# Optimization experiments

Hardware: AMD Instinct MI355X
Metric: run time of the kernel (lower is better)

The kernel has to match this reference:

```python
import jax, jax.numpy as jnp
import numpy as np


def _conv(x, w, b):
    # 3x3 stride-1 pad-1 conv, NCHW / OIHW
    y = jax.lax.conv_general_dilated(x, w, (1, 1), 'SAME',
                                     dimension_numbers=('NCHW', 'OIHW', 'NCHW'))
    return y + b[None, :, None, None]


def _lrelu(x):
    return jax.nn.leaky_relu(x, negative_slope=0.2)


def setup_inputs() -> dict:
    key = jax.random.key(0)
    ks = jax.random.split(key, 12)
    B, H, W = 64, 32, 32
    C, K, DH, OUT = 16, 10, 256, 784

    def w(k, shape, fan_in):
        return jax.random.normal(k, shape, jnp.float32) / np.sqrt(fan_in)

    inp = {
        'x':   jax.random.normal(ks[0], (B, 1, H, W), jnp.float32),
        # encoder convs
        'cw1': w(ks[1], (C, 1, 3, 3), 1 * 9),   'cb1': jnp.zeros((C,), jnp.float32),
        'cw2': w(ks[2], (C, C, 3, 3), C * 9),   'cb2': jnp.zeros((C,), jnp.float32),
        # 2 residual blocks, 2 convs each
        'r1w1': w(ks[3], (C, C, 3, 3), C * 9), 'r1b1': jnp.zeros((C,), jnp.float32),
        'r1w2': w(ks[4], (C, C, 3, 3), C * 9), 'r1b2': jnp.zeros((C,), jnp.float32),
        'r2w1': w(ks[5], (C, C, 3, 3), C * 9), 'r2b1': jnp.zeros((C,), jnp.float32),
        'r2w2': w(ks[6], (C, C, 3, 3), C * 9), 'r2b2': jnp.zeros((C,), jnp.float32),
        # VQ codebook (k=10 hardcoded in source, d = encoder channels)
        'codebook': jax.random.normal(ks[7], (K, C), jnp.float32),
        # decoder MLP 16 -> 256 -> 256 -> 784 (torch Linear layout: [out, in])
        'dw1': w(ks[8], (DH, C), C),     'db1': jnp.zeros((DH,), jnp.float32),
        'dw2': w(ks[9], (DH, DH), DH),   'db2': jnp.zeros((DH,), jnp.float32),
        'dw3': w(ks[10], (OUT, DH), DH), 'db3': jnp.zeros((OUT,), jnp.float32),
    }
    return inp


def reference(x, cw1, cb1, cw2, cb2,
              r1w1, r1b1, r1w2, r1b2, r2w1, r2b1, r2w2, r2b2,
              codebook, dw1, db1, dw2, db2, dw3, db3):
    # ---- encoder ----
    h = _lrelu(_conv(x, cw1, cb1))
    h = _lrelu(_conv(h, cw2, cb2))
    h = _lrelu(_conv(_lrelu(_conv(h, r1w1, r1b1)), r1w2, r1b2)) + h  # ResBlock 1
    h = _lrelu(_conv(_lrelu(_conv(h, r2w1, r2b1)), r2w2, r2b2)) + h  # ResBlock 2
    z_e = h  # [B, C, H, W]

    # ---- VQ: cdist^2 + argmin + gather ----
    B, C, H, W = z_e.shape
    x_flat = z_e.transpose(0, 2, 3, 1).reshape(-1, C)          # [N, C]
    d2 = (jnp.sum(x_flat ** 2, axis=1, keepdims=True)
          + jnp.sum(codebook ** 2, axis=1)[None, :]
          - 2.0 * x_flat @ codebook.T)                          # [N, K]
    idx = jnp.argmin(d2, axis=1)                                # [N]
    z_q = codebook[idx].reshape(B, H, W, C).transpose(0, 3, 1, 2)
    # straight-through (as written in source: value == z_e, grad flows via z_q)
    z_st = z_q + jax.lax.stop_gradient(z_e - z_q)               # [B, C, H, W]

    # ---- decoder: per-pixel MLP 16 -> 256 -> 256 -> 784 ----
    g = z_st.transpose(0, 2, 3, 1)                              # [B, H, W, C]
    g = _lrelu(g @ dw1.T + db1)
    g = _lrelu(g @ dw2.T + db2)
    x_recon = jax.nn.sigmoid(g @ dw3.T + db3)                   # [B, H, W, 784]
    return x_recon, z_e, z_st, z_q
```

## Files before the change

kernel.cpp:

```cpp
#include <hip/hip_runtime.h>

typedef __attribute__((ext_vector_type(8))) short bfrag;
typedef __attribute__((ext_vector_type(4))) float ffrag;

__device__ __forceinline__ float lrelu(float x) { return x > 0.f ? x : 0.2f * x; }

__device__ __forceinline__ short f2b(float f) {
    union { float f; unsigned u; } x; x.f = f;
    unsigned r = x.u + 0x7fffu + ((x.u >> 16) & 1u);
    return (short)(r >> 16);
}

__global__ __launch_bounds__(256) void prep_k(
    const float* __restrict__ dw1, const float* __restrict__ dw2, const float* __restrict__ dw3,
    const float* __restrict__ cw1, const float* __restrict__ cw2,
    const float* __restrict__ r1w1, const float* __restrict__ r1w2,
    const float* __restrict__ r2w1, const float* __restrict__ r2w2,
    short* __restrict__ dw1p, short* __restrict__ dw2b, short* __restrict__ dw3b,
    float* __restrict__ wtr)
{
    const int i = blockIdx.x * 256 + threadIdx.x;
    if (i < 65536)  dw2b[i] = f2b(dw2[i]);
    if (i < 200704) dw3b[i] = f2b(dw3[i]);
    if (i < 8192) {
        const int row = i >> 5, k = i & 31;
        dw1p[i] = (k < 16) ? f2b(dw1[row * 16 + k]) : (short)0;
    }
    if (i < 2304) {
        const int co = i & 15;
        const int q  = i >> 4;
        const int k  = q % 9;
        const int ci = q / 9;
        const int src = (co * 16 + ci) * 9 + k;
        wtr[2304 * 1 + i] = cw2 [src];
        wtr[2304 * 2 + i] = r1w1[src];
        wtr[2304 * 3 + i] = r1w2[src];
        wtr[2304 * 4 + i] = r2w1[src];
        wtr[2304 * 5 + i] = r2w2[src];
        if (ci == 0) wtr[i] = cw1[co * 9 + k];
    }
}

template<int CIN, int RIN, int ROUT, int HOUT, bool HASRES, int RRES, int HRES>
__device__ __forceinline__ void conv_stage(
    const float* __restrict__ in, float* __restrict__ out, const float* __restrict__ res,
    const float* __restrict__ wt, const float* __restrict__ bias, int r0, int t)
{
    const int lo = (r0 - HOUT > 0) ? r0 - HOUT : 0;
    const int hi = (r0 + 8 + HOUT < 32) ? r0 + 8 + HOUT : 32;
    const int base = r0 - HOUT;
    const int nlow = lo - base;
    const int hih  = hi - base;
    if (nlow > 0 || hih < ROUT) {
        const int nz = (nlow + (ROUT - hih)) * 36;
        for (int i = t; i < 16 * nz; i += 512) {
            const int ch = i / nz, rem = i % nz;
            int r = rem / 36; const int c = rem % 36;
            r = (r < nlow) ? r : (hih + (r - nlow));
            out[(ch * ROUT + r) * 36 + c] = 0.f;
        }
    }
    for (int i = t; i < 16 * ROUT * 2; i += 512) {
        const int ch = i / (ROUT * 2), rem = i % (ROUT * 2);
        out[(ch * ROUT + (rem >> 1)) * 36 + ((rem & 1) ? 33 : 0)] = 0.f;
    }

    const int n = (hi - lo) * 32;
    for (int u = t; u < n; u += 512) {
        const int row = lo + (u >> 5), col = u & 31;
        const int prin = row - r0 + HOUT;
        float acc[16];
        #pragma unroll
        for (int co = 0; co < 16; ++co) acc[co] = bias[co];
        for (int ci = 0; ci < CIN; ++ci) {
            const float* ip = in + (ci * RIN + prin) * 36 + col;
            float v[9];
            #pragma unroll
            for (int kh = 0; kh < 3; ++kh)
                #pragma unroll
                for (int kw = 0; kw < 3; ++kw) v[kh * 3 + kw] = ip[kh * 36 + kw];
            const float* wp = wt + ci * 144;
            #pragma unroll
            for (int k = 0; k < 9; ++k)
                #pragma unroll
                for (int co = 0; co < 16; ++co)
                    acc[co] = fmaf(v[k], wp[k * 16 + co], acc[co]);
        }
        const int pro = row - base;
        #pragma unroll
        for (int co = 0; co < 16; ++co) {
            float val = lrelu(acc[co]);
            if (HASRES) val += res[(co * RRES + (row - (r0 - HRES))) * 36 + col + 1];
            out[(co * ROUT + pro) * 36 + col + 1] = val;
        }
    }
    __syncthreads();
}

__global__ __launch_bounds__(512, 1) void enc_k(
    const float* __restrict__ x, const float* __restrict__ wtr,
    const float* __restrict__ cb1, const float* __restrict__ cb2,
    const float* __restrict__ r1b1, const float* __restrict__ r1b2,
    const float* __restrict__ r2b1, const float* __restrict__ r2b2,
    const float* __restrict__ cbk,
    float* __restrict__ ze, float* __restrict__ zq,
    float* __restrict__ zst, short* __restrict__ zstb)
{
    __shared__ float xb[20 * 36];
    __shared__ float Abuf[16 * 18 * 36];
    __shared__ float Bbuf[16 * 16 * 36];
    __shared__ float Cbuf[16 * 12 * 36];
    __shared__ float scb[160];
    __shared__ int   sbest[256];

    const int t  = threadIdx.x;
    const int b  = blockIdx.x >> 2;
    const int r0 = (blockIdx.x & 3) * 8;

    if (t < 160) scb[t] = cbk[t];
    for (int i = t; i < 720; i += 512) {
        const int r = i / 36, c = i % 36;
        const int rl = r0 - 6 + r, cl = c - 1;
        xb[i] = (rl >= 0 && rl < 32 && cl >= 0 && cl < 32)
              ? x[(size_t)b * 1024 + rl * 32 + cl] : 0.f;
    }
    __syncthreads();

    conv_stage<1,  20, 18, 5, false,  1, 0>(xb,   Abuf, nullptr, wtr,          cb1,  r0, t);
    conv_stage<16, 18, 16, 4, false,  1, 0>(Abuf, Bbuf, nullptr, wtr + 2304,   cb2,  r0, t);
    conv_stage<16, 16, 14, 3, false,  1, 0>(Bbuf, Abuf, nullptr, wtr + 4608,   r1b1, r0, t);
    conv_stage<16, 14, 12, 2, true,  16, 4>(Abuf, Cbuf, Bbuf,    wtr + 6912,   r1b2, r0, t);
    conv_stage<16, 12, 10, 1, false,  1, 0>(Cbuf, Abuf, nullptr, wtr + 9216,   r2b1, r0, t);
    conv_stage<16, 10,  8, 0, true,  12, 2>(Abuf, Bbuf, Cbuf,    wtr + 11520,  r2b2, r0, t);

    const size_t obase = (size_t)b * 16384 + r0 * 32;
    for (int i = t; i < 4096; i += 512) {
        const int c = i >> 8, px = i & 255;
        ze[obase + c * 1024 + px] = Bbuf[(c * 8 + (px >> 5)) * 36 + (px & 31) + 1];
    }
    if (t < 256) {
        const int r = t >> 5, col = t & 31;
        float xv[16]; float xx = 0.f;
        #pragma unroll
        for (int c = 0; c < 16; ++c) { xv[c] = Bbuf[(c * 8 + r) * 36 + col + 1]; xx += xv[c] * xv[c]; }
        int best = 0; float bestd = 1e30f;
        #pragma unroll
        for (int k = 0; k < 10; ++k) {
            float dot = 0.f, cn = 0.f;
            #pragma unroll
            for (int c = 0; c < 16; ++c) { const float cv = scb[k * 16 + c]; dot += xv[c] * cv; cn += cv * cv; }
            const float d2 = xx + cn - 2.f * dot;
            if (d2 < bestd) { bestd = d2; best = k; }
        }
        sbest[t] = best;
        unsigned pk[8];
        #pragma unroll
        for (int c = 0; c < 16; ++c) {
            const float q = scb[best * 16 + c];
            const float s = q + (xv[c] - q);
            const unsigned hb = (unsigned)(unsigned short)f2b(s);
            if (c & 1) pk[c >> 1] |= hb << 16; else pk[c >> 1] = hb;
        }
        const size_t n = (size_t)b * 1024 + (size_t)(r0 + r) * 32 + col;
        uint4* d = (uint4*)(zstb + n * 16);
        d[0] = make_uint4(pk[0], pk[1], pk[2], pk[3]);
        d[1] = make_uint4(pk[4], pk[5], pk[6], pk[7]);
    }
    __syncthreads();
    for (int i = t; i < 4096; i += 512) {
        const int c = i >> 8, px = i & 255;
        const float q  = scb[sbest[px] * 16 + c];
        const float xv = Bbuf[(c * 8 + (px >> 5)) * 36 + (px & 31) + 1];
        zq[obase + c * 1024 + px]  = q;
        zst[obase + c * 1024 + px] = q + (xv - q);
    }
}

__global__ __launch_bounds__(256, 2) void decoder_k(
    const short* __restrict__ zstb,
    const short* __restrict__ dw1p, const float* __restrict__ db1,
    const short* __restrict__ dw2b, const float* __restrict__ db2,
    const short* __restrict__ dw3b, const float* __restrict__ db3,
    float* __restrict__ xrec)
{
    __shared__ short g[4 * 8192];
    __shared__ short b3[2][4096];

    const int t    = threadIdx.x;
    const int lane = t & 63;
    const int wid  = t >> 6;
    const int lr   = lane & 15;
    const int lg   = lane >> 4;
    const int row0 = blockIdx.x * 128 + wid * 32;
    short* gw = g + wid * 8192;

    #define GB(row, kbyte) (((row) * 512 + (kbyte)) ^ (((row) & 7) << 4))

    auto stage2 = [&](short* dst, const short* src) {
        #pragma unroll
        for (int h = 0; h < 2; ++h) {
            const int L = h * 4096 + t * 16;
            const int S = L ^ (((L >> 9) & 7) << 4);
            __builtin_amdgcn_global_load_lds(
                (const __attribute__((address_space(1))) void*)((const char*)src + S),
                (__attribute__((address_space(3))) void*)((char*)dst + L), 16, 0, 0);
        }
    };

    stage2(&b3[0][0], dw2b);

    {
        bfrag A1[2];
        #pragma unroll
        for (int rt = 0; rt < 2; ++rt) {
            bfrag z;
            #pragma unroll
            for (int i = 0; i < 8; ++i) z[i] = 0;
            if (lg < 2)
                z = *(const bfrag*)&zstb[(size_t)(row0 + rt * 16 + lr) * 16 + lg * 8];
            A1[rt] = z;
        }
        #pragma unroll
        for (int ct = 0; ct < 16; ++ct) {
            const int col = ct * 16 + lr;
            const bfrag B = *(const bfrag*)&dw1p[col * 32 + lg * 8];
            const float bv = db1[col];
            ffrag acc[2];
            #pragma unroll
            for (int rt = 0; rt < 2; ++rt) {
                #pragma unroll
                for (int q = 0; q < 4; ++q) acc[rt][q] = bv;
                acc[rt] = __builtin_amdgcn_mfma_f32_16x16x32_bf16(A1[rt], B, acc[rt], 0, 0, 0);
            }
            #pragma unroll
            for (int rt = 0; rt < 2; ++rt)
                #pragma unroll
                for (int q = 0; q < 4; ++q) {
                    const int R = rt * 16 + lg * 4 + q;
                    *(short*)((char*)gw + GB(R, col * 2)) = f2b(lrelu(acc[rt][q]));
                }
        }
    }

    bfrag A[2][8];
    #pragma unroll
    for (int rt = 0; rt < 2; ++rt)
        #pragma unroll
        for (int kk = 0; kk < 8; ++kk)
            A[rt][kk] = *(const bfrag*)((char*)gw + GB(rt * 16 + lr, kk * 64 + lg * 16));

    __syncthreads();

    #pragma unroll 1
    for (int p = 0; p < 16; ++p) {
        if (p < 15) stage2(&b3[(p + 1) & 1][0], dw2b + (p + 1) * 4096);
        else        stage2(&b3[0][0],           dw3b);
        const char* bp = (const char*)&b3[p & 1][0];
        const int col = p * 16 + lr;
        bfrag Bf[8];
        #pragma unroll
        for (int kk = 0; kk < 8; ++kk)
            Bf[kk] = *(const bfrag*)(bp + (((lr * 512 + kk * 64 + lg * 16)) ^ ((lr & 7) << 4)));
        ffrag aE[2], aO[2];
        const float bv = db2[col];
        #pragma unroll
        for (int rt = 0; rt < 2; ++rt)
            #pragma unroll
            for (int q = 0; q < 4; ++q) { aE[rt][q] = bv; aO[rt][q] = 0.f; }
        #pragma unroll
        for (int kk = 0; kk < 8; kk += 2)
            #pragma unroll
            for (int rt = 0; rt < 2; ++rt) {
                aE[rt] = __builtin_amdgcn_mfma_f32_16x16x32_bf16(A[rt][kk],     Bf[kk],     aE[rt], 0, 0, 0);
                aO[rt] = __builtin_amdgcn_mfma_f32_16x16x32_bf16(A[rt][kk + 1], Bf[kk + 1], aO[rt], 0, 0, 0);
            }
        #pragma unroll
        for (int rt = 0; rt < 2; ++rt)
            #pragma unroll
            for (int q = 0; q < 4; ++q) {
                const int R = rt * 16 + lg * 4 + q;
                *(short*)((char*)gw + GB(R, col * 2)) = f2b(lrelu(aE[rt][q] + aO[rt][q]));
            }
        __syncthreads();
    }

    #pragma unroll
    for (int rt = 0; rt < 2; ++rt)
        #pragma unroll
        for (int kk = 0; kk < 8; ++kk)
            A[rt][kk] = *(const bfrag*)((char*)gw + GB(rt * 16 + lr, kk * 64 + lg * 16));

    float* slab = (float*)gw;

    #pragma unroll 1
    for (int p = 0; p < 49; ++p) {
        if (p < 48) stage2(&b3[(p + 1) & 1][0], dw3b + (p + 1) * 4096);
        const char* bp = (const char*)&b3[p & 1][0];
        const int col = p * 16 + lr;
        bfrag Bf[8];
        #pragma unroll
        for (int kk = 0; kk < 8; ++kk)
            Bf[kk] = *(const bfrag*)(bp + (((lr * 512 + kk * 64 + lg * 16)) ^ ((lr & 7) << 4)));
        ffrag aE[2], aO[2];
        const float bv = db3[col];
        #pragma unroll
        for (int rt = 0; rt < 2; ++rt)
            #pragma unroll
            for (int q = 0; q < 4; ++q) { aE[rt][q] = bv; aO[rt][q] = 0.f; }
        #pragma unroll
        for (int kk = 0; kk < 8; kk += 2)
            #pragma unroll
            for (int rt = 0; rt < 2; ++rt) {
                aE[rt] = __builtin_amdgcn_mfma_f32_16x16x32_bf16(A[rt][kk],     Bf[kk],     aE[rt], 0, 0, 0);
                aO[rt] = __builtin_amdgcn_mfma_f32_16x16x32_bf16(A[rt][kk + 1], Bf[kk + 1], aO[rt], 0, 0, 0);
            }
        const int ph = p & 1;
        #pragma unroll
        for (int rt = 0; rt < 2; ++rt)
            #pragma unroll
            for (int q = 0; q < 4; ++q) {
                const int R = rt * 16 + lg * 4 + q;
                const float v = aE[rt][q] + aO[rt][q];
                slab[R * 36 + ph * 16 + lr] = 1.f / (1.f + __expf(-v));
            }
        if (ph) {
            const int cb = (p - 1) * 16;
            #pragma unroll
            for (int f0 = 0; f0 < 4; ++f0) {
                const int f = f0 * 64 + lane;
                const int row = f >> 3, c4 = f & 7;
                const float4 v = *(const float4*)&slab[row * 36 + c4 * 4];
                *(float4*)&xrec[(size_t)(row0 + row) * 784 + cb + c4 * 4] = v;
            }
        }
        if (p == 48) {
            #pragma unroll
            for (int f0 = 0; f0 < 2; ++f0) {
                const int f = f0 * 64 + lane;
                const int row = f >> 2, c4 = f & 3;
                const float4 v = *(const float4*)&slab[row * 36 + c4 * 4];
                *(float4*)&xrec[(size_t)(row0 + row) * 784 + 768 + c4 * 4] = v;
            }
        }
        __syncthreads();
    }
    #undef GB
}

extern "C" void kernel_launch(void* const* d_in, const int* in_sizes, int n_in,
                              void* d_out, int out_size, void* d_ws, size_t ws_size,
                              hipStream_t stream) {
    const float* x    = (const float*)d_in[0];
    const float* cw1  = (const float*)d_in[1];
    const float* cb1  = (const float*)d_in[2];
    const float* cw2  = (const float*)d_in[3];
    const float* cb2  = (const float*)d_in[4];
    const float* r1w1 = (const float*)d_in[5];
    const float* r1b1 = (const float*)d_in[6];
    const float* r1w2 = (const float*)d_in[7];
    const float* r1b2 = (const float*)d_in[8];
    const float* r2w1 = (const float*)d_in[9];
    const float* r2b1 = (const float*)d_in[10];
    const float* r2w2 = (const float*)d_in[11];
    const float* r2b2 = (const float*)d_in[12];
    const float* cbk  = (const float*)d_in[13];
    const float* dw1  = (const float*)d_in[14];
    const float* db1  = (const float*)d_in[15];
    const float* dw2  = (const float*)d_in[16];
    const float* db2  = (const float*)d_in[17];
    const float* dw3  = (const float*)d_in[18];
    const float* db3  = (const float*)d_in[19];

    float* out  = (float*)d_out;
    float* xrec = out;
    float* ze   = out + 51380224;
    float* zst  = ze + 1048576;
    float* zq   = zst + 1048576;

    short* zstb = (short*)d_ws;
    short* dw2b = zstb + 1048576;
    short* dw3b = dw2b + 65536;
    short* dw1p = dw3b + 200704;
    float* wtr  = (float*)(dw1p + 8192);

    prep_k<<<784, 256, 0, stream>>>(dw1, dw2, dw3, cw1, cw2, r1w1, r1w2, r2w1, r2w2,
                                    dw1p, dw2b, dw3b, wtr);

    enc_k<<<256, 512, 0, stream>>>(x, wtr, cb1, cb2, r1b1, r1b2, r2b1, r2b2,
                                   cbk, ze, zq, zst, zstb);

    decoder_k<<<512, 256, 0, stream>>>(zstb, dw1p, db1, dw2b, db2, dw3b, db3, xrec);
}
```

Before: 156.0 us.

## Merge decoder layer loops into triple-buffered pipeline with 512-thread blocks

The decoder now runs 8 waves per block (256 rows) instead of 4, so each staged weight panel is shared by twice as many rows. The two GEMM loops for layers 2 and 3 are fused into one 65-step loop. Weight panels are triple-buffered with a two-step prefetch, and the full __syncthreads is replaced by a partial vmcnt wait plus a raw barrier. Biases are preloaded into shared memory. The intent is to halve weight traffic per row and hide the global-to-LDS load latency, at the cost of fewer blocks (256, one per CU) and a larger LDS footprint.

```diff
diff --git a/kernel.cpp b/kernel.cpp
--- a/kernel.cpp
+++ b/kernel.cpp
@@ -176,38 +176,39 @@
     }
 }
 
-__global__ __launch_bounds__(256, 2) void decoder_k(
+__global__ __launch_bounds__(512, 1) void decoder_k(
     const short* __restrict__ zstb,
     const short* __restrict__ dw1p, const float* __restrict__ db1,
     const short* __restrict__ dw2b, const float* __restrict__ db2,
     const short* __restrict__ dw3b, const float* __restrict__ db3,
     float* __restrict__ xrec)
 {
-    __shared__ short g[4 * 8192];
-    __shared__ short b3[2][4096];
+    __shared__ __align__(16) short g[8 * 8192];
+    __shared__ __align__(16) short pan[3][4096];
+    __shared__ float sb[1040];
 
     const int t    = threadIdx.x;
     const int lane = t & 63;
     const int wid  = t >> 6;
     const int lr   = lane & 15;
     const int lg   = lane >> 4;
-    const int row0 = blockIdx.x * 128 + wid * 32;
+    const int row0 = blockIdx.x * 256 + wid * 32;
     short* gw = g + wid * 8192;
 
     #define GB(row, kbyte) (((row) * 512 + (kbyte)) ^ (((row) & 7) << 4))
 
-    auto stage2 = [&](short* dst, const short* src) {
-        #pragma unroll
-        for (int h = 0; h < 2; ++h) {
-            const int L = h * 4096 + t * 16;
-            const int S = L ^ (((L >> 9) & 7) << 4);
-            __builtin_amdgcn_global_load_lds(
-                (const __attribute__((address_space(1))) void*)((const char*)src + S),
-                (__attribute__((address_space(3))) void*)((char*)dst + L), 16, 0, 0);
-        }
+    auto stage = [&](short* dst, const short* src) {
+        const int L = t * 16;
+        const int S = L ^ (((L >> 9) & 7) << 4);
+        __builtin_amdgcn_global_load_lds(
+            (const __attribute__((address_space(1))) void*)((const char*)src + S),
+            (__attribute__((address_space(3))) void*)((char*)dst + L), 16, 0, 0);
     };
 
-    stage2(&b3[0][0], dw2b);
+    stage(&pan[0][0], dw2b);
+    stage(&pan[1][0], dw2b + 4096);
+
+    for (int i = t; i < 1040; i += 512) sb[i] = (i < 256) ? db2[i] : db3[i - 256];
 
     {
         bfrag A1[2];
@@ -251,18 +252,36 @@
 
     __syncthreads();
 
+    float* slab = (float*)gw;
+
     #pragma unroll 1
-    for (int p = 0; p < 16; ++p) {
-        if (p < 15) stage2(&b3[(p + 1) & 1][0], dw2b + (p + 1) * 4096);
-        else        stage2(&b3[0][0],           dw3b);
-        const char* bp = (const char*)&b3[p & 1][0];
-        const int col = p * 16 + lr;
+    for (int p = 0; p < 65; ++p) {
+        if (p) {
+            asm volatile("s_waitcnt vmcnt(1)" ::: "memory");
+            __builtin_amdgcn_s_barrier();
+            __builtin_amdgcn_sched_barrier(0);
+        }
+        if (p == 16) {
+            #pragma unroll
+            for (int rt = 0; rt < 2; ++rt)
+                #pragma unroll
+                for (int kk = 0; kk < 8; ++kk)
+                    A[rt][kk] = *(const bfrag*)((char*)gw + GB(rt * 16 + lr, kk * 64 + lg * 16));
+        }
+        if (p + 2 <= 64) {
+            const int p2 = p + 2;
+            stage(&pan[p2 % 3][0], (p2 < 16) ? dw2b + p2 * 4096
+                                             : dw3b + (size_t)(p2 - 16) * 4096);
+        }
+
+        const char* bp = (const char*)&pan[p % 3][0];
         bfrag Bf[8];
         #pragma unroll
         for (int kk = 0; kk < 8; ++kk)
-            Bf[kk] = *(const bfrag*)(bp + (((lr * 512 + kk * 64 + lg * 16)) ^ ((lr & 7) << 4)));
+            Bf[kk] = *(const bfrag*)(bp + ((lr * 512 + kk * 64 + lg * 16) ^ ((lr & 7) << 4)));
+
         ffrag aE[2], aO[2];
-        const float bv = db2[col];
+        const float bv = sb[p * 16 + lr];
         #pragma unroll
         for (int rt = 0; rt < 2; ++rt)
             #pragma unroll
@@ -274,75 +293,47 @@
                 aE[rt] = __builtin_amdgcn_mfma_f32_16x16x32_bf16(A[rt][kk],     Bf[kk],     aE[rt], 0, 0, 0);
                 aO[rt] = __builtin_amdgcn_mfma_f32_16x16x32_bf16(A[rt][kk + 1], Bf[kk + 1], aO[rt], 0, 0, 0);
             }
-        #pragma unroll
-        for (int rt = 0; rt < 2; ++rt)
-            #pragma unroll
-            for (int q = 0; q < 4; ++q) {
-                const int R = rt * 16 + lg * 4 + q;
-                *(short*)((char*)gw + GB(R, col * 2)) = f2b(lrelu(aE[rt][q] + aO[rt][q]));
+
+        if (p < 16) {
+            const int col = p * 16 + lr;
+            #pragma unroll
+            for (int rt = 0; rt < 2; ++rt)
+                #pragma unroll
+                for (int q = 0; q < 4; ++q) {
+                    const int R = rt * 16 + lg * 4 + q;
+                    *(short*)((char*)gw + GB(R, col * 2)) = f2b(lrelu(aE[rt][q] + aO[rt][q]));
+                }
+        } else {
+            const int q3 = p - 16;
+            const int ph = q3 & 1;
+            #pragma unroll
+            for (int rt = 0; rt < 2; ++rt)
+                #pragma unroll
+                for (int q = 0; q < 4; ++q) {
+                    const int R = rt * 16 + lg * 4 + q;
+                    const float v = aE[rt][q] + aO[rt][q];
+                    slab[R * 36 + ph * 16 + lr] = 1.f / (1.f + __expf(-v));
+                }
+            if (ph) {
+                const int cb = (q3 - 1) * 16;
+                #pragma unroll
+                for (int f0 = 0; f0 < 4; ++f0) {
+                    const int f = f0 * 64 + lane;
+                    const int row = f >> 3, c4 = f & 7;
+                    const float4 v = *(const float4*)&slab[row * 36 + c4 * 4];
+                    *(float4*)&xrec[(size_t)(row0 + row) * 784 + cb + c4 * 4] = v;
+                }
             }
-        __syncthreads();
-    }
-
-    #pragma unroll
-    for (int rt = 0; rt < 2; ++rt)
-        #pragma unroll
-        for (int kk = 0; kk < 8; ++kk)
-            A[rt][kk] = *(const bfrag*)((char*)gw + GB(rt * 16 + lr, kk * 64 + lg * 16));
-
-    float* slab = (float*)gw;
-
-    #pragma unroll 1
-    for (int p = 0; p < 49; ++p) {
-        if (p < 48) stage2(&b3[(p + 1) & 1][0], dw3b + (p + 1) * 4096);
-        const char* bp = (const char*)&b3[p & 1][0];
-        const int col = p * 16 + lr;
-        bfrag Bf[8];
-        #pragma unroll
-        for (int kk = 0; kk < 8; ++kk)
-            Bf[kk] = *(const bfrag*)(bp + (((lr * 512 + kk * 64 + lg * 16)) ^ ((lr & 7) << 4)));
-        ffrag aE[2], aO[2];
-        const float bv = db3[col];
-        #pragma unroll
-        for (int rt = 0; rt < 2; ++rt)
-            #pragma unroll
-            for (int q = 0; q < 4; ++q) { aE[rt][q] = bv; aO[rt][q] = 0.f; }
-        #pragma unroll
-        for (int kk = 0; kk < 8; kk += 2)
-            #pragma unroll
-            for (int rt = 0; rt < 2; ++rt) {
-                aE[rt] = __builtin_amdgcn_mfma_f32_16x16x32_bf16(A[rt][kk],     Bf[kk],     aE[rt], 0, 0, 0);
-                aO[rt] = __builtin_amdgcn_mfma_f32_16x16x32_bf16(A[rt][kk + 1], Bf[kk + 1], aO[rt], 0, 0, 0);
+            if (q3 == 48) {
+                #pragma unroll
+                for (int f0 = 0; f0 < 2; ++f0) {
+                    const int f = f0 * 64 + lane;
+                    const int row = f >> 2, c4 = f & 3;
+                    const float4 v = *(const float4*)&slab[row * 36 + c4 * 4];
+                    *(float4*)&xrec[(size_t)(row0 + row) * 784 + 768 + c4 * 4] = v;
+                }
             }
-        const int ph = p & 1;
-        #pragma unroll
-        for (int rt = 0; rt < 2; ++rt)
-            #pragma unroll
-            for (int q = 0; q < 4; ++q) {
-                const int R = rt * 16 + lg * 4 + q;
-                const float v = aE[rt][q] + aO[rt][q];
-                slab[R * 36 + ph * 16 + lr] = 1.f / (1.f + __expf(-v));
-            }
-        if (ph) {
-            const int cb = (p - 1) * 16;
-            #pragma unroll
-            for (int f0 = 0; f0 < 4; ++f0) {
-                const int f = f0 * 64 + lane;
-                const int row = f >> 3, c4 = f & 7;
-                const float4 v = *(const float4*)&slab[row * 36 + c4 * 4];
-                *(float4*)&xrec[(size_t)(row0 + row) * 784 + cb + c4 * 4] = v;
-            }
-        }
-        if (p == 48) {
-            #pragma unroll
-            for (int f0 = 0; f0 < 2; ++f0) {
-                const int f = f0 * 64 + lane;
-                const int row = f >> 2, c4 = f & 3;
-                const float4 v = *(const float4*)&slab[row * 36 + c4 * 4];
-                *(float4*)&xrec[(size_t)(row0 + row) * 784 + 768 + c4 * 4] = v;
-            }
-        }
-        __syncthreads();
+        }
     }
     #undef GB
 }
@@ -389,5 +380,5 @@
     enc_k<<<256, 512, 0, stream>>>(x, wtr, cb1, cb2, r1b1, r1b2, r2b1, r2b2,
                                    cbk, ze, zq, zst, zstb);
 
-    decoder_k<<<512, 256, 0, stream>>>(zstb, dw1p, db1, dw2b, db2, dw3b, db3, xrec);
-}
+    decoder_k<<<256, 512, 0, stream>>>(zstb, dw1p, db1, dw2b, db2, dw3b, db3, xrec);
+}
```

Result: slower. 160.3 us (+2.7%).
